# Performance work log

Measured on AMD Instinct MI355X. Metric: run time of the kernel, lower is better.

Reference implementation:

```python
import jax, jax.numpy as jnp
import numpy as np

D = 32  # embedding_dimension (TGN default memory_dimension == embedding_dimension)


def time_encode(t, w, b):
    # TGN TimeEncode: cos(t * w + b); t: [E] -> [E, D]
    return jnp.cos(t[:, None] * w[None, :] + b[None, :])


def setup_inputs() -> dict:
    key = jax.random.key(0)
    ks = jax.random.split(key, 24)
    N, B, E, F, NE = 1_000_000, 262_144, 1_048_576, 64, 500_000
    inp = {}
    # per-node-type memory tables (Mailbox memory)
    inp["mem_user"] = jax.random.normal(ks[0], (N, D), jnp.float32)
    inp["mem_item"] = jax.random.normal(ks[1], (N, D), jnp.float32)
    # active event node ids per type (memory lookup indices)
    inp["node_ids_user"] = jax.random.randint(ks[2], (B,), 0, N, jnp.int32)
    inp["node_ids_item"] = jax.random.randint(ks[3], (B,), 0, N, jnp.int32)
    # heterogeneous edge lists: user->item and item->user (indices into the B active nodes)
    inp["edge_src_ui"] = jax.random.randint(ks[4], (E,), 0, B, jnp.int32)
    inp["edge_dst_ui"] = jax.random.randint(ks[5], (E,), 0, B, jnp.int32)
    inp["edge_src_iu"] = jax.random.randint(ks[6], (E,), 0, B, jnp.int32)
    inp["edge_dst_iu"] = jax.random.randint(ks[7], (E,), 0, B, jnp.int32)
    inp["edge_idx_ui"] = jax.random.randint(ks[8], (E,), 0, NE, jnp.int32)
    inp["edge_idx_iu"] = jax.random.randint(ks[9], (E,), 0, NE, jnp.int32)
    inp["edge_rel_times_ui"] = jax.random.uniform(ks[10], (E,), jnp.float32) * 1000.0
    inp["edge_rel_times_iu"] = jax.random.uniform(ks[11], (E,), jnp.float32) * 1000.0
    inp["edge_feature"] = jax.random.normal(ks[12], (NE, F), jnp.float32)
    # per-node-type Linear(D, D, bias=False) == self.lin[node_type]
    s = 1.0 / np.sqrt(D)
    inp["W_user"] = jax.random.normal(ks[13], (D, D), jnp.float32) * s
    inp["W_item"] = jax.random.normal(ks[14], (D, D), jnp.float32) * s
    # per-edge-type Linear(F, D) == self.edge_feature_linear[edge_type]
    se = 1.0 / np.sqrt(F)
    inp["We_ui"] = jax.random.normal(ks[15], (F, D), jnp.float32) * se
    inp["be_ui"] = jnp.zeros((D,), jnp.float32)
    inp["We_iu"] = jax.random.normal(ks[16], (F, D), jnp.float32) * se
    inp["be_iu"] = jnp.zeros((D,), jnp.float32)
    # TimeEncode params (standard TGN init: 1/10^linspace)
    inp["time_w"] = jnp.asarray(1.0 / (10.0 ** np.linspace(0, 9, D)), jnp.float32)
    inp["time_b"] = jnp.zeros((D,), jnp.float32)
    # decoder(2*D -> 64 -> 16 -> 1), drop=0
    inp["dec_W1"] = jax.random.normal(ks[17], (2 * D, 64), jnp.float32) * (1.0 / np.sqrt(2 * D))
    inp["dec_b1"] = jnp.zeros((64,), jnp.float32)
    inp["dec_W2"] = jax.random.normal(ks[18], (64, 16), jnp.float32) * 0.125
    inp["dec_b2"] = jnp.zeros((16,), jnp.float32)
    inp["dec_W3"] = jax.random.normal(ks[19], (16, 1), jnp.float32) * 0.25
    inp["dec_b3"] = jnp.zeros((1,), jnp.float32)
    return inp


def reference(mem_user, mem_item, edge_feature, edge_rel_times_ui, edge_rel_times_iu,
              W_user, W_item, We_ui, be_ui, We_iu, be_iu, time_w, time_b,
              dec_W1, dec_b1, dec_W2, dec_b2, dec_W3, dec_b3,
              node_ids_user, node_ids_item, edge_src_ui, edge_dst_ui,
              edge_src_iu, edge_dst_iu, edge_idx_ui, edge_idx_iu):
    B = node_ids_user.shape[0]
    # memory lookup + per-node-type linear (self.lin[node_type], bias=False)
    h_user = mem_user[node_ids_user] @ W_user   # [B, D]
    h_item = mem_item[node_ids_item] @ W_item   # [B, D]
    # heterogeneous message passing: src memory + edge-feature linear + time encoding,
    # scattered (segment_sum) onto destination nodes per edge type
    msg_ui = (h_user[edge_src_ui]
              + edge_feature[edge_idx_ui] @ We_ui + be_ui
              + time_encode(edge_rel_times_ui, time_w, time_b))  # [E, D]
    agg_item = jax.ops.segment_sum(msg_ui, edge_dst_ui, num_segments=B)
    msg_iu = (h_item[edge_src_iu]
              + edge_feature[edge_idx_iu] @ We_iu + be_iu
              + time_encode(edge_rel_times_iu, time_w, time_b))  # [E, D]
    agg_user = jax.ops.segment_sum(msg_iu, edge_dst_iu, num_segments=B)
    hu = jax.nn.relu(h_user + agg_user)
    hi = jax.nn.relu(h_item + agg_item)
    # decoder `distance` on concatenated pair embeddings (2*D -> 64 -> 16 -> 1), drop=0
    z = jnp.concatenate([hu, hi], axis=-1)      # [B, 2D]
    x = jax.nn.relu(z @ dec_W1 + dec_b1)
    x = jax.nn.relu(x @ dec_W2 + dec_b2)
    return x @ dec_W3 + dec_b3                   # [B, 1]
```

## Files before the change

kernel.cpp:

```cpp
#include <hip/hip_runtime.h>

#define DEV __device__ __forceinline__

typedef __attribute__((ext_vector_type(8))) short short8;
typedef __attribute__((ext_vector_type(16))) float float16;

DEV unsigned short f2bf(float x) {
    unsigned u = __float_as_uint(x);
    unsigned r = (u + 0x7FFFu + ((u >> 16) & 1u)) >> 16;
    return (unsigned short)r;
}
DEV float bf2f(unsigned short v) {
    return __uint_as_float(((unsigned)v) << 16);
}
DEV float fastcos(float x) {
    float r = x * 0.15915494309189535f;
    r = r - floorf(r);
    return __builtin_amdgcn_cosf(r);
}

__global__ void prep_kernel(const float* __restrict__ W_user, const float* __restrict__ W_item,
                            const float* __restrict__ We_ui, const float* __restrict__ be_ui,
                            const float* __restrict__ We_iu, const float* __restrict__ be_iu,
                            const float* __restrict__ dW1, const float* __restrict__ dW2,
                            float* __restrict__ Wt_user, float* __restrict__ Wt_item,
                            unsigned short* __restrict__ Wb, float* __restrict__ bc,
                            float* __restrict__ W1t, float* __restrict__ W2t) {
    int t = threadIdx.x;
    for (int i = t; i < 1024; i += 256) {
        int k = i / 32, d = i % 32;
        Wt_user[d * 32 + k] = W_user[i];
        Wt_item[d * 32 + k] = W_item[i];
    }
    for (int i = t; i < 4096; i += 256) {
        int kt   = i >> 10;
        int rem  = i & 1023;
        int n2   = rem >> 9;
        int rem2 = rem & 511;
        int l    = rem2 >> 3;
        int ii   = rem2 & 7;
        int k = kt * 16 + (l >> 5) * 8 + ii;
        int n = (l & 31);
        float v = n2 ? We_iu[k * 32 + n] : We_ui[k * 32 + n];
        Wb[i] = f2bf(v);
    }
    for (int i = t; i < 64; i += 256)
        bc[i] = (i < 32) ? be_ui[i] : be_iu[i - 32];
    for (int i = t; i < 4096; i += 256) {
        int j = i / 64, k = i % 64;
        W1t[i] = dW1[k * 64 + j];
    }
    for (int i = t; i < 1024; i += 256) {
        int c = i / 64, j = i % 64;
        W2t[i] = dW2[j * 16 + c];
    }
}

__global__ __launch_bounds__(256) void node_linear_kernel(
        const float* __restrict__ mem, const int* __restrict__ ids,
        const float* __restrict__ Wt, float* __restrict__ h, int B) {
    int r = blockIdx.x * 256 + threadIdx.x;
    if (r >= B) return;
    int id = ids[r];
    const float4* m4 = (const float4*)(mem + (size_t)id * 32);
    float m[32];
#pragma unroll
    for (int q = 0; q < 8; ++q) {
        float4 v = m4[q];
        m[4 * q + 0] = v.x; m[4 * q + 1] = v.y; m[4 * q + 2] = v.z; m[4 * q + 3] = v.w;
    }
    float* hr = h + (size_t)r * 32;
    for (int db = 0; db < 8; ++db) {
        float acc[4];
#pragma unroll
        for (int u = 0; u < 4; ++u) {
            const float* wr = Wt + (size_t)(db * 4 + u) * 32;
            float a = 0.f;
#pragma unroll
            for (int k = 0; k < 32; ++k) a = fmaf(m[k], wr[k], a);
            acc[u] = a;
        }
        float4 o; o.x = acc[0]; o.y = acc[1]; o.z = acc[2]; o.w = acc[3];
        *(float4*)(hr + db * 4) = o;
    }
}

__global__ __launch_bounds__(256) void proj_mfma_kernel(
        const float* __restrict__ feat, const unsigned short* __restrict__ Wb,
        const float* __restrict__ bc, unsigned short* __restrict__ proj, int NE) {
    __shared__ unsigned short lds[128 * 72];
    const int lane = threadIdx.x & 63;
    const int wave = threadIdx.x >> 6;
    const int col  = lane & 31;
    const int half = lane >> 5;

    short8 bfrag[8];
    const short8* wb8 = (const short8*)Wb;
#pragma unroll
    for (int f = 0; f < 8; ++f) bfrag[f] = wb8[f * 64 + lane];

    int r = blockIdx.x * 128 + wave * 32 + col;
    if (r >= NE) r = NE - 1;
    const float* fr = feat + (size_t)r * 64 + half * 8;
    short8 afrag[4];
#pragma unroll
    for (int t = 0; t < 4; ++t) {
        float4 a = *(const float4*)(fr + t * 16);
        float4 b = *(const float4*)(fr + t * 16 + 4);
        short8 s;
        s[0] = (short)f2bf(a.x); s[1] = (short)f2bf(a.y);
        s[2] = (short)f2bf(a.z); s[3] = (short)f2bf(a.w);
        s[4] = (short)f2bf(b.x); s[5] = (short)f2bf(b.y);
        s[6] = (short)f2bf(b.z); s[7] = (short)f2bf(b.w);
        afrag[t] = s;
    }

    float16 acc0, acc1;
    float b0 = bc[col], b1 = bc[32 + col];
#pragma unroll
    for (int i = 0; i < 16; ++i) { acc0[i] = b0; acc1[i] = b1; }
#pragma unroll
    for (int t = 0; t < 4; ++t) {
        acc0 = __builtin_amdgcn_mfma_f32_32x32x16_bf16(afrag[t], bfrag[t * 2 + 0], acc0, 0, 0, 0);
        acc1 = __builtin_amdgcn_mfma_f32_32x32x16_bf16(afrag[t], bfrag[t * 2 + 1], acc1, 0, 0, 0);
    }

#pragma unroll
    for (int reg = 0; reg < 16; ++reg) {
        int rl = wave * 32 + (reg & 3) + 8 * (reg >> 2) + 4 * half;
        lds[rl * 72 + col]      = f2bf(acc0[reg]);
        lds[rl * 72 + 32 + col] = f2bf(acc1[reg]);
    }
    __syncthreads();

    int trow = threadIdx.x >> 1, thalf = threadIdx.x & 1;
    int grow = blockIdx.x * 128 + trow;
    if (grow < NE) {
        const uint4* lsrc = (const uint4*)(lds + trow * 72 + thalf * 32);
        uint4* gdst = (uint4*)(proj + (size_t)grow * 64 + thalf * 32);
#pragma unroll
        for (int s = 0; s < 4; ++s) gdst[s] = lsrc[s];
    }
}

__global__ __launch_bounds__(256) void hist_kernel(
        const int* __restrict__ dst_ui, const int* __restrict__ dst_iu,
        int* __restrict__ cnt, int E, int B) {
    int ge = blockIdx.x * 256 + threadIdx.x;
    if (ge >= 2 * E) return;
    int d = (ge < E) ? dst_ui[ge] : (dst_iu[ge - E] + B);
    atomicAdd(cnt + d, 1);
}

__global__ __launch_bounds__(256) void scan1_kernel(
        const int* __restrict__ cnt, int* __restrict__ base,
        int* __restrict__ part, int n) {
    __shared__ int sh[256];
    int t = threadIdx.x;
    int i0 = blockIdx.x * 1024 + t * 4;
    int c0 = (i0 + 0 < n) ? cnt[i0 + 0] : 0;
    int c1 = (i0 + 1 < n) ? cnt[i0 + 1] : 0;
    int c2 = (i0 + 2 < n) ? cnt[i0 + 2] : 0;
    int c3 = (i0 + 3 < n) ? cnt[i0 + 3] : 0;
    int s = c0 + c1 + c2 + c3;
    sh[t] = s; __syncthreads();
    for (int off = 1; off < 256; off <<= 1) {
        int v = sh[t];
        int a = (t >= off) ? sh[t - off] : 0;
        __syncthreads();
        sh[t] = v + a;
        __syncthreads();
    }
    int excl = sh[t] - s;
    if (t == 255) part[blockIdx.x] = sh[255];
    if (i0 + 0 < n) base[i0 + 0] = excl; excl += c0;
    if (i0 + 1 < n) base[i0 + 1] = excl; excl += c1;
    if (i0 + 2 < n) base[i0 + 2] = excl; excl += c2;
    if (i0 + 3 < n) base[i0 + 3] = excl;
}

__global__ __launch_bounds__(256) void scan2_kernel(int* __restrict__ part, int n) {
    __shared__ int sh[256];
    int t = threadIdx.x;
    int i0 = t * 16;
    int c[16];
#pragma unroll
    for (int q = 0; q < 16; ++q) c[q] = (i0 + q < n) ? part[i0 + q] : 0;
    int s = 0;
#pragma unroll
    for (int q = 0; q < 16; ++q) s += c[q];
    sh[t] = s; __syncthreads();
    for (int off = 1; off < 256; off <<= 1) {
        int v = sh[t];
        int a = (t >= off) ? sh[t - off] : 0;
        __syncthreads();
        sh[t] = v + a;
        __syncthreads();
    }
    int excl = sh[t] - s;
#pragma unroll
    for (int q = 0; q < 16; ++q) { if (i0 + q < n) part[i0 + q] = excl; excl += c[q]; }
}

__global__ __launch_bounds__(256) void scan3_kernel(
        int* __restrict__ base, const int* __restrict__ part, int n) {
    int i = blockIdx.x * 256 + threadIdx.x;
    if (i < n) base[i] += part[i >> 10];
}

__global__ __launch_bounds__(256) void scatter_kernel(
        const int* __restrict__ src_ui, const int* __restrict__ eidx_ui,
        const float* __restrict__ rt_ui, const int* __restrict__ dst_ui,
        const int* __restrict__ src_iu, const int* __restrict__ eidx_iu,
        const float* __restrict__ rt_iu, const int* __restrict__ dst_iu,
        int* __restrict__ base, int4* __restrict__ edata, int E, int B) {
    int ge = blockIdx.x * 256 + threadIdx.x;
    if (ge >= 2 * E) return;
    int s, ix, d; float tv;
    if (ge < E) {
        s = src_ui[ge]; ix = eidx_ui[ge]; tv = rt_ui[ge]; d = dst_ui[ge];
    } else {
        int e = ge - E;
        s = src_iu[e]; ix = eidx_iu[e]; tv = rt_iu[e]; d = dst_iu[e] + B;
    }
    int pos = atomicAdd(base + d, 1);
    edata[pos] = make_int4(s, ix, __float_as_int(tv), 0);
}

__global__ __launch_bounds__(256) void agg_kernel(
        const int4* __restrict__ edata, const int* __restrict__ base,
        const float* __restrict__ h_user, const float* __restrict__ h_item,
        const unsigned short* __restrict__ proj,
        float* __restrict__ agg_user, float* __restrict__ agg_item,
        const float* __restrict__ tw, const float* __restrict__ tb, int B) {
    int g = threadIdx.x >> 5, d = threadIdx.x & 31;
    int n = blockIdx.x * 8 + g;
    if (n >= 2 * B) return;
    int type = (n >= B);
    int b1 = base[n];
    int b0 = n ? base[n - 1] : 0;
    const float* h = type ? h_item : h_user;
    const unsigned short* pr = proj + (type ? 32 : 0) + d;
    float twd = tw[d], tbd = tb[d];
    float acc = 0.f;
    if (b0 < b1) {
        int4 ed = edata[b0];
        for (int j = b0; j < b1; ++j) {
            int4 cur = ed;
            if (j + 1 < b1) ed = edata[j + 1];
            float pv = bf2f(pr[(size_t)cur.y * 64]);
            float c  = fastcos(fmaf(__int_as_float(cur.z), twd, tbd));
            acc += h[(size_t)cur.x * 32 + d] + pv + c;
        }
    }
    if (type) agg_user[(size_t)(n - B) * 32 + d] = acc;
    else      agg_item[(size_t)n * 32 + d] = acc;
}

__global__ __launch_bounds__(256) void decoder_kernel(
        const float* __restrict__ h_user, const float* __restrict__ h_item,
        const float* __restrict__ agg_user, const float* __restrict__ agg_item,
        const float* __restrict__ W1t, const float* __restrict__ b1,
        const float* __restrict__ W2t, const float* __restrict__ b2,
        const float* __restrict__ W3, const float* __restrict__ b3,
        float* __restrict__ out, int B) {
    int i = blockIdx.x * 256 + threadIdx.x;
    if (i >= B) return;
    float z[64];
    {
        const float4* a4 = (const float4*)(h_user + (size_t)i * 32);
        const float4* b4 = (const float4*)(agg_user + (size_t)i * 32);
#pragma unroll
        for (int q = 0; q < 8; ++q) {
            float4 a = a4[q], b = b4[q];
            z[4 * q + 0] = fmaxf(a.x + b.x, 0.f);
            z[4 * q + 1] = fmaxf(a.y + b.y, 0.f);
            z[4 * q + 2] = fmaxf(a.z + b.z, 0.f);
            z[4 * q + 3] = fmaxf(a.w + b.w, 0.f);
        }
    }
    {
        const float4* a4 = (const float4*)(h_item + (size_t)i * 32);
        const float4* b4 = (const float4*)(agg_item + (size_t)i * 32);
#pragma unroll
        for (int q = 0; q < 8; ++q) {
            float4 a = a4[q], b = b4[q];
            z[32 + 4 * q + 0] = fmaxf(a.x + b.x, 0.f);
            z[32 + 4 * q + 1] = fmaxf(a.y + b.y, 0.f);
            z[32 + 4 * q + 2] = fmaxf(a.z + b.z, 0.f);
            z[32 + 4 * q + 3] = fmaxf(a.w + b.w, 0.f);
        }
    }
    float x2[16];
#pragma unroll
    for (int c = 0; c < 16; ++c) x2[c] = b2[c];
    for (int jb = 0; jb < 8; ++jb) {
        float a[8];
#pragma unroll
        for (int u = 0; u < 8; ++u) {
            int j = jb * 8 + u;
            const float* wr = W1t + (size_t)j * 64;
            float acc = b1[j];
#pragma unroll
            for (int k = 0; k < 64; ++k) acc = fmaf(z[k], wr[k], acc);
            a[u] = fmaxf(acc, 0.f);
        }
#pragma unroll
        for (int c = 0; c < 16; ++c) {
            const float* w2r = W2t + (size_t)c * 64 + jb * 8;
            float acc = x2[c];
#pragma unroll
            for (int u = 0; u < 8; ++u) acc = fmaf(a[u], w2r[u], acc);
            x2[c] = acc;
        }
    }
    float o = b3[0];
#pragma unroll
    for (int c = 0; c < 16; ++c) o = fmaf(fmaxf(x2[c], 0.f), W3[c], o);
    out[i] = o;
}

extern "C" void kernel_launch(void* const* d_in, const int* in_sizes, int n_in,
                              void* d_out, int out_size, void* d_ws, size_t ws_size,
                              hipStream_t stream) {
    const float* mem_user = (const float*)d_in[0];
    const float* mem_item = (const float*)d_in[1];
    const int*   ids_user = (const int*)d_in[2];
    const int*   ids_item = (const int*)d_in[3];
    const int*   src_ui   = (const int*)d_in[4];
    const int*   dst_ui   = (const int*)d_in[5];
    const int*   src_iu   = (const int*)d_in[6];
    const int*   dst_iu   = (const int*)d_in[7];
    const int*   eidx_ui  = (const int*)d_in[8];
    const int*   eidx_iu  = (const int*)d_in[9];
    const float* rt_ui    = (const float*)d_in[10];
    const float* rt_iu    = (const float*)d_in[11];
    const float* feat     = (const float*)d_in[12];
    const float* W_user   = (const float*)d_in[13];
    const float* W_item   = (const float*)d_in[14];
    const float* We_ui    = (const float*)d_in[15];
    const float* be_ui    = (const float*)d_in[16];
    const float* We_iu    = (const float*)d_in[17];
    const float* be_iu    = (const float*)d_in[18];
    const float* tw       = (const float*)d_in[19];
    const float* tb       = (const float*)d_in[20];
    const float* dW1      = (const float*)d_in[21];
    const float* db1      = (const float*)d_in[22];
    const float* dW2      = (const float*)d_in[23];
    const float* db2      = (const float*)d_in[24];
    const float* dW3      = (const float*)d_in[25];
    const float* db3      = (const float*)d_in[26];

    const int B  = in_sizes[2];
    const int E  = in_sizes[4];
    const int NE = in_sizes[12] / 64;
    const int NB2 = 2 * B;

    float* w = (float*)d_ws;
    const size_t hsz = (size_t)B * 32;
    float* h_user   = w;
    float* h_item   = h_user + hsz;
    float* agg_user = h_item + hsz;
    float* agg_item = agg_user + hsz;
    float* Wt_user  = agg_item + hsz;
    float* Wt_item  = Wt_user + 1024;
    unsigned short* Wb = (unsigned short*)(Wt_item + 1024);
    float* bc       = (float*)(Wb + 4096);
    float* W1t      = bc + 64;
    float* W2t      = W1t + 4096;
    unsigned short* proj = (unsigned short*)(W2t + 1024);
    int* cnt  = (int*)(proj + (size_t)NE * 64);
    int* base = cnt + NB2;
    int* part = base + NB2;
    int4* edata = (int4*)(part + 4096);

    prep_kernel<<<1, 256, 0, stream>>>(W_user, W_item, We_ui, be_ui, We_iu, be_iu, dW1, dW2,
                                       Wt_user, Wt_item, Wb, bc, W1t, W2t);
    hipMemsetAsync(cnt, 0, (size_t)NB2 * sizeof(int), stream);
    node_linear_kernel<<<(B + 255) / 256, 256, 0, stream>>>(mem_user, ids_user, Wt_user, h_user, B);
    node_linear_kernel<<<(B + 255) / 256, 256, 0, stream>>>(mem_item, ids_item, Wt_item, h_item, B);
    proj_mfma_kernel<<<(NE + 127) / 128, 256, 0, stream>>>(feat, Wb, bc, proj, NE);

    int e2blocks = (2 * E + 255) / 256;
    hist_kernel<<<e2blocks, 256, 0, stream>>>(dst_ui, dst_iu, cnt, E, B);
    int nblk1 = (NB2 + 1023) / 1024;
    scan1_kernel<<<nblk1, 256, 0, stream>>>(cnt, base, part, NB2);
    scan2_kernel<<<1, 256, 0, stream>>>(part, nblk1);
    scan3_kernel<<<(NB2 + 255) / 256, 256, 0, stream>>>(base, part, NB2);
    scatter_kernel<<<e2blocks, 256, 0, stream>>>(src_ui, eidx_ui, rt_ui, dst_ui,
                                                 src_iu, eidx_iu, rt_iu, dst_iu,
                                                 base, edata, E, B);
    agg_kernel<<<(NB2 + 7) / 8, 256, 0, stream>>>(edata, base, h_user, h_item, proj,
                                                  agg_user, agg_item, tw, tb, B);
    decoder_kernel<<<(B + 255) / 256, 256, 0, stream>>>(h_user, h_item, agg_user, agg_item,
                                                        W1t, db1, W2t, db2, dW3, db3,
                                                        (float*)d_out, B);
}
```

Before: 917.2 us.

## Replace CSR bucketing with atomic linked lists per destination node

Drops the histogram, three-stage prefix scan and counting scatter used to group edges by destination. A single link kernel now pushes each edge onto a per-node list head with atomicExch, storing the previous head in the edge record. The aggregation kernel walks these lists instead of contiguous CSR ranges. This removes several launches and a full pass over the destination arrays. In exchange, aggregation chases dependent pointers into scattered edge records with no prefetch, and the summation order is no longer deterministic.

```diff
diff --git a/kernel.cpp b/kernel.cpp
--- a/kernel.cpp
+++ b/kernel.cpp
@@ -143,77 +143,12 @@
     }
 }
 
-__global__ __launch_bounds__(256) void hist_kernel(
-        const int* __restrict__ dst_ui, const int* __restrict__ dst_iu,
-        int* __restrict__ cnt, int E, int B) {
-    int ge = blockIdx.x * 256 + threadIdx.x;
-    if (ge >= 2 * E) return;
-    int d = (ge < E) ? dst_ui[ge] : (dst_iu[ge - E] + B);
-    atomicAdd(cnt + d, 1);
-}
-
-__global__ __launch_bounds__(256) void scan1_kernel(
-        const int* __restrict__ cnt, int* __restrict__ base,
-        int* __restrict__ part, int n) {
-    __shared__ int sh[256];
-    int t = threadIdx.x;
-    int i0 = blockIdx.x * 1024 + t * 4;
-    int c0 = (i0 + 0 < n) ? cnt[i0 + 0] : 0;
-    int c1 = (i0 + 1 < n) ? cnt[i0 + 1] : 0;
-    int c2 = (i0 + 2 < n) ? cnt[i0 + 2] : 0;
-    int c3 = (i0 + 3 < n) ? cnt[i0 + 3] : 0;
-    int s = c0 + c1 + c2 + c3;
-    sh[t] = s; __syncthreads();
-    for (int off = 1; off < 256; off <<= 1) {
-        int v = sh[t];
-        int a = (t >= off) ? sh[t - off] : 0;
-        __syncthreads();
-        sh[t] = v + a;
-        __syncthreads();
-    }
-    int excl = sh[t] - s;
-    if (t == 255) part[blockIdx.x] = sh[255];
-    if (i0 + 0 < n) base[i0 + 0] = excl; excl += c0;
-    if (i0 + 1 < n) base[i0 + 1] = excl; excl += c1;
-    if (i0 + 2 < n) base[i0 + 2] = excl; excl += c2;
-    if (i0 + 3 < n) base[i0 + 3] = excl;
-}
-
-__global__ __launch_bounds__(256) void scan2_kernel(int* __restrict__ part, int n) {
-    __shared__ int sh[256];
-    int t = threadIdx.x;
-    int i0 = t * 16;
-    int c[16];
-#pragma unroll
-    for (int q = 0; q < 16; ++q) c[q] = (i0 + q < n) ? part[i0 + q] : 0;
-    int s = 0;
-#pragma unroll
-    for (int q = 0; q < 16; ++q) s += c[q];
-    sh[t] = s; __syncthreads();
-    for (int off = 1; off < 256; off <<= 1) {
-        int v = sh[t];
-        int a = (t >= off) ? sh[t - off] : 0;
-        __syncthreads();
-        sh[t] = v + a;
-        __syncthreads();
-    }
-    int excl = sh[t] - s;
-#pragma unroll
-    for (int q = 0; q < 16; ++q) { if (i0 + q < n) part[i0 + q] = excl; excl += c[q]; }
-}
-
-__global__ __launch_bounds__(256) void scan3_kernel(
-        int* __restrict__ base, const int* __restrict__ part, int n) {
-    int i = blockIdx.x * 256 + threadIdx.x;
-    if (i < n) base[i] += part[i >> 10];
-}
-
-__global__ __launch_bounds__(256) void scatter_kernel(
-        const int* __restrict__ src_ui, const int* __restrict__ eidx_ui,
-        const float* __restrict__ rt_ui, const int* __restrict__ dst_ui,
-        const int* __restrict__ src_iu, const int* __restrict__ eidx_iu,
-        const float* __restrict__ rt_iu, const int* __restrict__ dst_iu,
-        int* __restrict__ base, int4* __restrict__ edata, int E, int B) {
+__global__ __launch_bounds__(256) void link_kernel(
+        const int* __restrict__ src_ui, const int* __restrict__ dst_ui,
+        const int* __restrict__ eidx_ui, const float* __restrict__ rt_ui,
+        const int* __restrict__ src_iu, const int* __restrict__ dst_iu,
+        const int* __restrict__ eidx_iu, const float* __restrict__ rt_iu,
+        int* __restrict__ head, int4* __restrict__ edata, int E, int B) {
     int ge = blockIdx.x * 256 + threadIdx.x;
     if (ge >= 2 * E) return;
     int s, ix, d; float tv;
@@ -223,12 +158,12 @@
         int e = ge - E;
         s = src_iu[e]; ix = eidx_iu[e]; tv = rt_iu[e]; d = dst_iu[e] + B;
     }
-    int pos = atomicAdd(base + d, 1);
-    edata[pos] = make_int4(s, ix, __float_as_int(tv), 0);
+    int nxt = atomicExch(head + d, ge);
+    edata[ge] = make_int4(s, ix, __float_as_int(tv), nxt);
 }
 
 __global__ __launch_bounds__(256) void agg_kernel(
-        const int4* __restrict__ edata, const int* __restrict__ base,
+        const int4* __restrict__ edata, const int* __restrict__ head,
         const float* __restrict__ h_user, const float* __restrict__ h_item,
         const unsigned short* __restrict__ proj,
         float* __restrict__ agg_user, float* __restrict__ agg_item,
@@ -237,21 +172,17 @@
     int n = blockIdx.x * 8 + g;
     if (n >= 2 * B) return;
     int type = (n >= B);
-    int b1 = base[n];
-    int b0 = n ? base[n - 1] : 0;
     const float* h = type ? h_item : h_user;
     const unsigned short* pr = proj + (type ? 32 : 0) + d;
     float twd = tw[d], tbd = tb[d];
     float acc = 0.f;
-    if (b0 < b1) {
-        int4 ed = edata[b0];
-        for (int j = b0; j < b1; ++j) {
-            int4 cur = ed;
-            if (j + 1 < b1) ed = edata[j + 1];
-            float pv = bf2f(pr[(size_t)cur.y * 64]);
-            float c  = fastcos(fmaf(__int_as_float(cur.z), twd, tbd));
-            acc += h[(size_t)cur.x * 32 + d] + pv + c;
-        }
+    int e = head[n];
+    while (e >= 0) {
+        int4 cur = edata[e];
+        float pv = bf2f(pr[(size_t)cur.y * 64]);
+        float c  = fastcos(fmaf(__int_as_float(cur.z), twd, tbd));
+        acc += h[(size_t)cur.x * 32 + d] + pv + c;
+        e = cur.w;
     }
     if (type) agg_user[(size_t)(n - B) * 32 + d] = acc;
     else      agg_item[(size_t)n * 32 + d] = acc;
@@ -369,28 +300,22 @@
     float* W1t      = bc + 64;
     float* W2t      = W1t + 4096;
     unsigned short* proj = (unsigned short*)(W2t + 1024);
-    int* cnt  = (int*)(proj + (size_t)NE * 64);
-    int* base = cnt + NB2;
-    int* part = base + NB2;
-    int4* edata = (int4*)(part + 4096);
+    int* head = (int*)(proj + (size_t)NE * 64);
+    int4* edata = (int4*)(head + NB2);
 
     prep_kernel<<<1, 256, 0, stream>>>(W_user, W_item, We_ui, be_ui, We_iu, be_iu, dW1, dW2,
                                        Wt_user, Wt_item, Wb, bc, W1t, W2t);
-    hipMemsetAsync(cnt, 0, (size_t)NB2 * sizeof(int), stream);
+    hipMemsetAsync(head, 0xFF, (size_t)NB2 * sizeof(int), stream);
+
+    proj_mfma_kernel<<<(NE + 127) / 128, 256, 0, stream>>>(feat, Wb, bc, proj, NE);
     node_linear_kernel<<<(B + 255) / 256, 256, 0, stream>>>(mem_user, ids_user, Wt_user, h_user, B);
     node_linear_kernel<<<(B + 255) / 256, 256, 0, stream>>>(mem_item, ids_item, Wt_item, h_item, B);
-    proj_mfma_kernel<<<(NE + 127) / 128, 256, 0, stream>>>(feat, Wb, bc, proj, NE);
 
     int e2blocks = (2 * E + 255) / 256;
-    hist_kernel<<<e2blocks, 256, 0, stream>>>(dst_ui, dst_iu, cnt, E, B);
-    int nblk1 = (NB2 + 1023) / 1024;
-    scan1_kernel<<<nblk1, 256, 0, stream>>>(cnt, base, part, NB2);
-    scan2_kernel<<<1, 256, 0, stream>>>(part, nblk1);
-    scan3_kernel<<<(NB2 + 255) / 256, 256, 0, stream>>>(base, part, NB2);
-    scatter_kernel<<<e2blocks, 256, 0, stream>>>(src_ui, eidx_ui, rt_ui, dst_ui,
-                                                 src_iu, eidx_iu, rt_iu, dst_iu,
-                                                 base, edata, E, B);
-    agg_kernel<<<(NB2 + 7) / 8, 256, 0, stream>>>(edata, base, h_user, h_item, proj,
+    link_kernel<<<e2blocks, 256, 0, stream>>>(src_ui, dst_ui, eidx_ui, rt_ui,
+                                              src_iu, dst_iu, eidx_iu, rt_iu,
+                                              head, edata, E, B);
+    agg_kernel<<<(NB2 + 7) / 8, 256, 0, stream>>>(edata, head, h_user, h_item, proj,
                                                   agg_user, agg_item, tw, tb, B);
     decoder_kernel<<<(B + 255) / 256, 256, 0, stream>>>(h_user, h_item, agg_user, agg_item,
                                                         W1t, db1, W2t, db2, dW3, db3,
```

New measurement: 815.2 us. 11.1% less time.
